# Kernel optimization log

Hardware: AMD Instinct MI355X
Metric: run time of the kernel (lower is better)

## Reference

```python
import jax, jax.numpy as jnp
import numpy as np

KS = 7          # kernel size (ks in __init__)
PAD = KS // 2   # 'same' padding, stride = 1


def _parapool(x, scale, mode):
    """Semifield pooling with parabolic structuring element.

    mode='min': erosion  out = min_{z in window} ( x[p+z] + ||z||^2 * scale_c )
    mode='max': dilation out = max_{z in window} ( x[p+z] - ||z||^2 * scale_c )
    x: [B, C, H, W], scale: [C] (learnable, per-channel).
    Padding uses the semifield identity (+inf for min, -inf for max).
    """
    B, C, H, W = x.shape
    if mode == "min":
        fill, agg, sign = jnp.inf, jnp.minimum, 1.0
    else:
        fill, agg, sign = -jnp.inf, jnp.maximum, -1.0
    xp = jnp.pad(x, ((0, 0), (0, 0), (PAD, PAD), (PAD, PAD)),
                 constant_values=fill)
    out = None
    # loop over the fixed ks*ks offsets (49 shifted adds + min/max; no unfold)
    for i in range(KS):
        for j in range(KS):
            p = float((i - PAD) ** 2 + (j - PAD) ** 2)  # parabola ||z||^2
            w = sign * p * scale[:, None, None]          # [C,1,1]
            cand = xp[:, :, i:i + H, j:j + W] + w
            out = cand if out is None else agg(out, cand)
    return out


def setup_inputs() -> dict:
    key = jax.random.key(0)
    k1, = jax.random.split(key, 1)
    x = jax.random.normal(k1, (8, 64, 256, 256), dtype=jnp.float32)
    # initial_scale = 1.0 per __init__ default
    scale_min = jnp.ones((64,), dtype=jnp.float32)
    scale_max = jnp.ones((64,), dtype=jnp.float32)
    return {"x": x, "scale_min": scale_min, "scale_max": scale_max}


def reference(x, scale_min, scale_max):
    y = _parapool(x, scale_min, "min")   # min-plus erosion
    y = _parapool(y, scale_max, "max")   # max-plus dilation
    return y
```

## Files before the change

kernel.cpp:

```cpp
#include <hip/hip_runtime.h>


#define TILE 64
#define NTH  256

#define XS   80
#define HMS  72
#define ES   72
#define HXS  68

#define XR   76
#define ER   70

__global__ __launch_bounds__(NTH) void parapool_fused(
    const float* __restrict__ x,
    const float* __restrict__ scale_min,
    const float* __restrict__ scale_max,
    float* __restrict__ out,
    int B, int C, int H, int W)
{
    const int tilesW = W / TILE;
    const int tilesH = H / TILE;
    int blk = blockIdx.x;
    const int tx = blk % tilesW; blk /= tilesW;
    const int ty = blk % tilesH; blk /= tilesH;
    const int bc = blk;
    const int ch = bc % C;

    const float sn = scale_min[ch];
    const float sx = scale_max[ch];
    const float w1n = 1.0f*sn, w2n = 4.0f*sn, w3n = 9.0f*sn;
    const float w1x = 1.0f*sx, w2x = 4.0f*sx, w3x = 9.0f*sx;

    const float* __restrict__ xp = x   + (size_t)bc * H * W;
    float* __restrict__       op = out + (size_t)bc * H * W;
    const int r0 = ty * TILE, c0 = tx * TILE;
    const int tid = threadIdx.x;
    const float INF = __builtin_inff();

    __shared__ float sA[XR * XS];
    __shared__ float sB[XR * HMS];
    float* Xl   = sA;
    float* Hmin = sB;
    float* El   = sA;
    float* Hmax = sB;

    for (int t = tid; t < XR * 20; t += NTH) {
        const int r = t / 20, q = t - r * 20;
        const int gr = r0 - 6 + r;
        const int gc = c0 - 8 + 4 * q;
        float4 v;
        if ((unsigned)gr < (unsigned)H && (unsigned)gc < (unsigned)(W - 3)) {
            v = *(const float4*)&xp[gr * W + gc];
        } else {
            float* e = (float*)&v;
            #pragma unroll
            for (int k = 0; k < 4; ++k) {
                const int g = gc + k;
                e[k] = ((unsigned)gr < (unsigned)H && (unsigned)g < (unsigned)W)
                         ? xp[gr * W + g] : INF;
            }
        }
        *(float4*)&Xl[r * XS + 4 * q] = v;
    }
    __syncthreads();

    for (int t = tid; t < XR * 18; t += NTH) {
        const int r = t / 18, g = t - r * 18;
        const float* px = &Xl[r * XS + 4 * g];
        const float4 a = *(const float4*)px;
        const float4 b = *(const float4*)(px + 4);
        const float4 cc = *(const float4*)(px + 8);
        const float xx[12] = {a.x,a.y,a.z,a.w, b.x,b.y,b.z,b.w, cc.x,cc.y,cc.z,cc.w};
        float4 o; float* oo = (float*)&o;
        #pragma unroll
        for (int m = 0; m < 4; ++m) {
            const float v0 = xx[m+4];
            const float m1 = fminf(xx[m+3], xx[m+5]) + w1n;
            const float m2 = fminf(xx[m+2], xx[m+6]) + w2n;
            const float m3 = fminf(xx[m+1], xx[m+7]) + w3n;
            oo[m] = fminf(fminf(v0, m1), fminf(m2, m3));
        }
        *(float4*)&Hmin[r * HMS + 4 * g] = o;
    }
    __syncthreads();

    if (tid < 252) {
        const int rg = tid / 18, g = tid - rg * 18;
        float4 win[11];
        #pragma unroll
        for (int i = 0; i < 11; ++i)
            win[i] = *(const float4*)&Hmin[(5 * rg + i) * HMS + 4 * g];
        #pragma unroll
        for (int s = 0; s < 5; ++s) {
            const int er = -3 + 5 * rg + s;
            const int gr = r0 + er;
            float4 o; float* oo = (float*)&o;
            #pragma unroll
            for (int m = 0; m < 4; ++m) {
                const float v0 = ((const float*)&win[s+3])[m];
                const float m1 = fminf(((const float*)&win[s+2])[m],
                                       ((const float*)&win[s+4])[m]) + w1n;
                const float m2 = fminf(((const float*)&win[s+1])[m],
                                       ((const float*)&win[s+5])[m]) + w2n;
                const float m3 = fminf(((const float*)&win[s+0])[m],
                                       ((const float*)&win[s+6])[m]) + w3n;
                float e = fminf(fminf(v0, m1), fminf(m2, m3));
                const int gc = c0 - 4 + 4 * g + m;
                const bool in = ((unsigned)gr < (unsigned)H) &&
                                ((unsigned)gc < (unsigned)W);
                oo[m] = in ? e : -INF;
            }
            *(float4*)&El[(er + 3) * ES + 4 * g] = o;
        }
    }
    __syncthreads();

    for (int t = tid; t < ER * 16; t += NTH) {
        const int r = t / 16, g = t - r * 16;
        const float* pe = &El[r * ES + 4 * g];
        const float4 a = *(const float4*)pe;
        const float4 b = *(const float4*)(pe + 4);
        const float4 cc = *(const float4*)(pe + 8);
        const float xx[12] = {a.x,a.y,a.z,a.w, b.x,b.y,b.z,b.w, cc.x,cc.y,cc.z,cc.w};
        float4 o; float* oo = (float*)&o;
        #pragma unroll
        for (int m = 0; m < 4; ++m) {
            const float v0 = xx[m+4];
            const float m1 = fmaxf(xx[m+3], xx[m+5]) - w1x;
            const float m2 = fmaxf(xx[m+2], xx[m+6]) - w2x;
            const float m3 = fmaxf(xx[m+1], xx[m+7]) - w3x;
            oo[m] = fmaxf(fmaxf(v0, m1), fmaxf(m2, m3));
        }
        *(float4*)&Hmax[r * HXS + 4 * g] = o;
    }
    __syncthreads();

    {
        const int rg = tid / 16, g = tid & 15;
        float4 win[10];
        #pragma unroll
        for (int i = 0; i < 10; ++i)
            win[i] = *(const float4*)&Hmax[(4 * rg + i) * HXS + 4 * g];
        #pragma unroll
        for (int s = 0; s < 4; ++s) {
            float4 o; float* oo = (float*)&o;
            #pragma unroll
            for (int m = 0; m < 4; ++m) {
                const float v0 = ((const float*)&win[s+3])[m];
                const float m1 = fmaxf(((const float*)&win[s+2])[m],
                                       ((const float*)&win[s+4])[m]) - w1x;
                const float m2 = fmaxf(((const float*)&win[s+1])[m],
                                       ((const float*)&win[s+5])[m]) - w2x;
                const float m3 = fmaxf(((const float*)&win[s+0])[m],
                                       ((const float*)&win[s+6])[m]) - w3x;
                oo[m] = fmaxf(fmaxf(v0, m1), fmaxf(m2, m3));
            }
            *(float4*)&op[(size_t)(r0 + 4 * rg + s) * W + (c0 + 4 * g)] = o;
        }
    }
}

extern "C" void kernel_launch(void* const* d_in, const int* in_sizes, int n_in,
                              void* d_out, int out_size, void* d_ws, size_t ws_size,
                              hipStream_t stream) {
    const float* x    = (const float*)d_in[0];
    const float* smin = (const float*)d_in[1];
    const float* smax = (const float*)d_in[2];
    float* out = (float*)d_out;

    const int C = in_sizes[1];
    const int H = 256, W = 256;
    const int B = in_sizes[0] / (C * H * W);

    const int tiles = (H / TILE) * (W / TILE);
    dim3 grid(B * C * tiles);
    parapool_fused<<<grid, NTH, 0, stream>>>(x, smin, smax, out, B, C, H, W);
}
```

Baseline: 285.9 us.

## Replace shared-memory tiles with per-wavefront row streaming and shuffle-based horizontal passes

```diff
diff --git a/kernel.cpp b/kernel.cpp
--- a/kernel.cpp
+++ b/kernel.cpp
@@ -1,162 +1,133 @@
 #include <hip/hip_runtime.h>
 
 
-#define TILE 64
+#define ROWS 32
+#define HH   256
+#define WW   256
 #define NTH  256
 
-#define XS   80
-#define HMS  72
-#define ES   72
-#define HXS  68
+__device__ __forceinline__ float4 f4s(float v) { return float4{v, v, v, v}; }
 
-#define XR   76
-#define ER   70
+__device__ __forceinline__ float4 f4min(float4 a, float4 b) {
+    return float4{fminf(a.x,b.x), fminf(a.y,b.y), fminf(a.z,b.z), fminf(a.w,b.w)};
+}
+__device__ __forceinline__ float4 f4max(float4 a, float4 b) {
+    return float4{fmaxf(a.x,b.x), fmaxf(a.y,b.y), fmaxf(a.z,b.z), fmaxf(a.w,b.w)};
+}
+__device__ __forceinline__ float4 f4add(float4 a, float s) {
+    return float4{a.x+s, a.y+s, a.z+s, a.w+s};
+}
 
-__global__ __launch_bounds__(NTH) void parapool_fused(
+template<bool IS_MIN>
+__device__ __forceinline__ float4 hpass(float4 v, float w1, float w2, float w3,
+                                        int lane) {
+    const float EDGE = IS_MIN ? __builtin_inff() : -__builtin_inff();
+    float ly = __shfl_up(v.y, 1, 64);
+    float lz = __shfl_up(v.z, 1, 64);
+    float lw = __shfl_up(v.w, 1, 64);
+    float rx = __shfl_down(v.x, 1, 64);
+    float ry = __shfl_down(v.y, 1, 64);
+    float rz = __shfl_down(v.z, 1, 64);
+    if (lane == 0)  { ly = EDGE; lz = EDGE; lw = EDGE; }
+    if (lane == 63) { rx = EDGE; ry = EDGE; rz = EDGE; }
+    const float win[10] = {ly, lz, lw, v.x, v.y, v.z, v.w, rx, ry, rz};
+    float o[4];
+#pragma unroll
+    for (int m = 0; m < 4; ++m) {
+        const float v0 = win[m+3];
+        if (IS_MIN) {
+            const float m1 = fminf(win[m+2], win[m+4]) + w1;
+            const float m2 = fminf(win[m+1], win[m+5]) + w2;
+            const float m3 = fminf(win[m],   win[m+6]) + w3;
+            o[m] = fminf(fminf(v0, m1), fminf(m2, m3));
+        } else {
+            const float m1 = fmaxf(win[m+2], win[m+4]) - w1;
+            const float m2 = fmaxf(win[m+1], win[m+5]) - w2;
+            const float m3 = fmaxf(win[m],   win[m+6]) - w3;
+            o[m] = fmaxf(fmaxf(v0, m1), fmaxf(m2, m3));
+        }
+    }
+    return float4{o[0], o[1], o[2], o[3]};
+}
+
+template<bool IS_MIN>
+__device__ __forceinline__ float4 vpass(const float4 w[7], float w1, float w2,
+                                        float w3) {
+    if (IS_MIN) {
+        const float4 m1 = f4add(f4min(w[2], w[4]),  w1);
+        const float4 m2 = f4add(f4min(w[1], w[5]),  w2);
+        const float4 m3 = f4add(f4min(w[0], w[6]),  w3);
+        return f4min(f4min(w[3], m1), f4min(m2, m3));
+    } else {
+        const float4 m1 = f4add(f4max(w[2], w[4]), -w1);
+        const float4 m2 = f4add(f4max(w[1], w[5]), -w2);
+        const float4 m3 = f4add(f4max(w[0], w[6]), -w3);
+        return f4max(f4max(w[3], m1), f4max(m2, m3));
+    }
+}
+
+__device__ __forceinline__ float4 loadrow(const float* __restrict__ xp, int gr,
+                                          int lane) {
+    if ((unsigned)gr < (unsigned)HH)
+        return *(const float4*)&xp[gr * WW + lane * 4];
+    return f4s(__builtin_inff());
+}
+
+__global__ __launch_bounds__(NTH) void parapool_stream(
     const float* __restrict__ x,
     const float* __restrict__ scale_min,
     const float* __restrict__ scale_max,
-    float* __restrict__ out,
-    int B, int C, int H, int W)
+    float* __restrict__ out, int C)
 {
-    const int tilesW = W / TILE;
-    const int tilesH = H / TILE;
-    int blk = blockIdx.x;
-    const int tx = blk % tilesW; blk /= tilesW;
-    const int ty = blk % tilesH; blk /= tilesH;
-    const int bc = blk;
+    const int lane = threadIdx.x & 63;
+    const int wv   = threadIdx.x >> 6;
+    const int gid  = blockIdx.x * 4 + wv;
+    const int sPerImg = HH / ROWS;
+    const int bc = gid / sPerImg;
+    const int st = gid - bc * sPerImg;
     const int ch = bc % C;
+    const int rs = st * ROWS;
 
     const float sn = scale_min[ch];
     const float sx = scale_max[ch];
     const float w1n = 1.0f*sn, w2n = 4.0f*sn, w3n = 9.0f*sn;
     const float w1x = 1.0f*sx, w2x = 4.0f*sx, w3x = 9.0f*sx;
 
-    const float* __restrict__ xp = x   + (size_t)bc * H * W;
-    float* __restrict__       op = out + (size_t)bc * H * W;
-    const int r0 = ty * TILE, c0 = tx * TILE;
-    const int tid = threadIdx.x;
+    const float* __restrict__ xp = x   + (size_t)bc * (HH * WW);
+    float* __restrict__       op = out + (size_t)bc * (HH * WW);
+
     const float INF = __builtin_inff();
+    float4 hw[7], mw[7];
+#pragma unroll
+    for (int k = 0; k < 7; ++k) { hw[k] = f4s(INF); mw[k] = f4s(-INF); }
 
-    __shared__ float sA[XR * XS];
-    __shared__ float sB[XR * HMS];
-    float* Xl   = sA;
-    float* Hmin = sB;
-    float* El   = sA;
-    float* Hmax = sB;
+    float4 xnext = loadrow(xp, rs - 6, lane);
 
-    for (int t = tid; t < XR * 20; t += NTH) {
-        const int r = t / 20, q = t - r * 20;
-        const int gr = r0 - 6 + r;
-        const int gc = c0 - 8 + 4 * q;
-        float4 v;
-        if ((unsigned)gr < (unsigned)H && (unsigned)gc < (unsigned)(W - 3)) {
-            v = *(const float4*)&xp[gr * W + gc];
-        } else {
-            float* e = (float*)&v;
-            #pragma unroll
-            for (int k = 0; k < 4; ++k) {
-                const int g = gc + k;
-                e[k] = ((unsigned)gr < (unsigned)H && (unsigned)g < (unsigned)W)
-                         ? xp[gr * W + g] : INF;
-            }
-        }
-        *(float4*)&Xl[r * XS + 4 * q] = v;
-    }
-    __syncthreads();
+#pragma unroll 2
+    for (int it = 0; it < ROWS + 12; ++it) {
+        const int gr = rs - 6 + it;
+        const float4 xv = xnext;
+        xnext = loadrow(xp, gr + 1, lane);
 
-    for (int t = tid; t < XR * 18; t += NTH) {
-        const int r = t / 18, g = t - r * 18;
-        const float* px = &Xl[r * XS + 4 * g];
-        const float4 a = *(const float4*)px;
-        const float4 b = *(const float4*)(px + 4);
-        const float4 cc = *(const float4*)(px + 8);
-        const float xx[12] = {a.x,a.y,a.z,a.w, b.x,b.y,b.z,b.w, cc.x,cc.y,cc.z,cc.w};
-        float4 o; float* oo = (float*)&o;
-        #pragma unroll
-        for (int m = 0; m < 4; ++m) {
-            const float v0 = xx[m+4];
-            const float m1 = fminf(xx[m+3], xx[m+5]) + w1n;
-            const float m2 = fminf(xx[m+2], xx[m+6]) + w2n;
-            const float m3 = fminf(xx[m+1], xx[m+7]) + w3n;
-            oo[m] = fminf(fminf(v0, m1), fminf(m2, m3));
-        }
-        *(float4*)&Hmin[r * HMS + 4 * g] = o;
-    }
-    __syncthreads();
+        const float4 hm = hpass<true>(xv, w1n, w2n, w3n, lane);
+#pragma unroll
+        for (int k = 0; k < 6; ++k) hw[k] = hw[k+1];
+        hw[6] = hm;
 
-    if (tid < 252) {
-        const int rg = tid / 18, g = tid - rg * 18;
-        float4 win[11];
-        #pragma unroll
-        for (int i = 0; i < 11; ++i)
-            win[i] = *(const float4*)&Hmin[(5 * rg + i) * HMS + 4 * g];
-        #pragma unroll
-        for (int s = 0; s < 5; ++s) {
-            const int er = -3 + 5 * rg + s;
-            const int gr = r0 + er;
-            float4 o; float* oo = (float*)&o;
-            #pragma unroll
-            for (int m = 0; m < 4; ++m) {
-                const float v0 = ((const float*)&win[s+3])[m];
-                const float m1 = fminf(((const float*)&win[s+2])[m],
-                                       ((const float*)&win[s+4])[m]) + w1n;
-                const float m2 = fminf(((const float*)&win[s+1])[m],
-                                       ((const float*)&win[s+5])[m]) + w2n;
-                const float m3 = fminf(((const float*)&win[s+0])[m],
-                                       ((const float*)&win[s+6])[m]) + w3n;
-                float e = fminf(fminf(v0, m1), fminf(m2, m3));
-                const int gc = c0 - 4 + 4 * g + m;
-                const bool in = ((unsigned)gr < (unsigned)H) &&
-                                ((unsigned)gc < (unsigned)W);
-                oo[m] = in ? e : -INF;
-            }
-            *(float4*)&El[(er + 3) * ES + 4 * g] = o;
-        }
-    }
-    __syncthreads();
+        const int er = gr - 3;
+        float4 E;
+        if ((unsigned)er < (unsigned)HH)
+            E = vpass<true>(hw, w1n, w2n, w3n);
+        else
+            E = f4s(-INF);
+        const float4 hx = hpass<false>(E, w1x, w2x, w3x, lane);
+#pragma unroll
+        for (int k = 0; k < 6; ++k) mw[k] = mw[k+1];
+        mw[6] = hx;
 
-    for (int t = tid; t < ER * 16; t += NTH) {
-        const int r = t / 16, g = t - r * 16;
-        const float* pe = &El[r * ES + 4 * g];
-        const float4 a = *(const float4*)pe;
-        const float4 b = *(const float4*)(pe + 4);
-        const float4 cc = *(const float4*)(pe + 8);
-        const float xx[12] = {a.x,a.y,a.z,a.w, b.x,b.y,b.z,b.w, cc.x,cc.y,cc.z,cc.w};
-        float4 o; float* oo = (float*)&o;
-        #pragma unroll
-        for (int m = 0; m < 4; ++m) {
-            const float v0 = xx[m+4];
-            const float m1 = fmaxf(xx[m+3], xx[m+5]) - w1x;
-            const float m2 = fmaxf(xx[m+2], xx[m+6]) - w2x;
-            const float m3 = fmaxf(xx[m+1], xx[m+7]) - w3x;
-            oo[m] = fmaxf(fmaxf(v0, m1), fmaxf(m2, m3));
-        }
-        *(float4*)&Hmax[r * HXS + 4 * g] = o;
-    }
-    __syncthreads();
-
-    {
-        const int rg = tid / 16, g = tid & 15;
-        float4 win[10];
-        #pragma unroll
-        for (int i = 0; i < 10; ++i)
-            win[i] = *(const float4*)&Hmax[(4 * rg + i) * HXS + 4 * g];
-        #pragma unroll
-        for (int s = 0; s < 4; ++s) {
-            float4 o; float* oo = (float*)&o;
-            #pragma unroll
-            for (int m = 0; m < 4; ++m) {
-                const float v0 = ((const float*)&win[s+3])[m];
-                const float m1 = fmaxf(((const float*)&win[s+2])[m],
-                                       ((const float*)&win[s+4])[m]) - w1x;
-                const float m2 = fmaxf(((const float*)&win[s+1])[m],
-                                       ((const float*)&win[s+5])[m]) - w2x;
-                const float m3 = fmaxf(((const float*)&win[s+0])[m],
-                                       ((const float*)&win[s+6])[m]) - w3x;
-                oo[m] = fmaxf(fmaxf(v0, m1), fmaxf(m2, m3));
-            }
-            *(float4*)&op[(size_t)(r0 + 4 * rg + s) * W + (c0 + 4 * g)] = o;
+        if (it >= 12) {
+            const float4 o = vpass<false>(mw, w1x, w2x, w3x);
+            *(float4*)&op[(gr - 6) * WW + lane * 4] = o;
         }
     }
 }
@@ -170,10 +141,9 @@
     float* out = (float*)d_out;
 
     const int C = in_sizes[1];
-    const int H = 256, W = 256;
-    const int B = in_sizes[0] / (C * H * W);
+    const int B = in_sizes[0] / (C * HH * WW);
 
-    const int tiles = (H / TILE) * (W / TILE);
-    dim3 grid(B * C * tiles);
-    parapool_fused<<<grid, NTH, 0, stream>>>(x, smin, smax, out, B, C, H, W);
+    const int totalStrips = B * C * (HH / ROWS);
+    dim3 grid(totalStrips / 4);
+    parapool_stream<<<grid, NTH, 0, stream>>>(x, smin, smax, out, C);
 }
```

New measurement: 250.2 us. -12.5%, faster.
